# Kernel optimization log

Measured on AMD Instinct MI355X. Metric: run time of the kernel, lower is better.

## Reference

```python
import jax, jax.numpy as jnp
import numpy as np

N = 20000
E = 320000
CIN = 16
COUT = 16
D = 4
RADIUS = 0.5


def setup_inputs() -> dict:
    key = jax.random.key(0)
    k1, k2, k3, k4 = jax.random.split(key, 4)
    positions = jax.random.uniform(k1, (N, 3), dtype=jnp.float32)
    features = jax.random.normal(k2, (N, CIN), dtype=jnp.float32)
    filters = jax.random.normal(k3, (D, D, D, CIN, COUT), dtype=jnp.float32)
    edge_index = jax.random.randint(k4, (2, E), 0, N, dtype=jnp.int32)
    return {"positions": positions, "features": features,
            "filters": filters, "edge_index": edge_index}


def _trilinear(filters, gc):
    # Replicates torch grid_sample(align_corners=True) semantics used by the
    # module: grid coord (x,y,z) indexes spatial dims (W,H,D), i.e. gc[:,0]
    # samples filter axis 2, gc[:,1] axis 1, gc[:,2] axis 0.
    Dres = filters.shape[0]
    a, b, c = gc[:, 2], gc[:, 1], gc[:, 0]  # axes 0, 1, 2 of filters
    a0f, b0f, c0f = jnp.floor(a), jnp.floor(b), jnp.floor(c)
    a0 = jnp.clip(a0f.astype(jnp.int32), 0, Dres - 1)
    b0 = jnp.clip(b0f.astype(jnp.int32), 0, Dres - 1)
    c0 = jnp.clip(c0f.astype(jnp.int32), 0, Dres - 1)
    a1 = jnp.minimum(a0 + 1, Dres - 1)
    b1 = jnp.minimum(b0 + 1, Dres - 1)
    c1 = jnp.minimum(c0 + 1, Dres - 1)
    ad = (a - a0f)[:, None, None]  # (E,1,1)
    bd = (b - b0f)[:, None, None]
    cd = (c - c0f)[:, None, None]

    g = lambda i, j, k: filters[i, j, k]  # (E, CIN, COUT) gather
    f00 = g(a0, b0, c0) * (1 - cd) + g(a0, b0, c1) * cd
    f01 = g(a0, b1, c0) * (1 - cd) + g(a0, b1, c1) * cd
    f10 = g(a1, b0, c0) * (1 - cd) + g(a1, b0, c1) * cd
    f11 = g(a1, b1, c0) * (1 - cd) + g(a1, b1, c1) * cd
    f0 = f00 * (1 - bd) + f01 * bd
    f1 = f10 * (1 - bd) + f11 * bd
    return f0 * (1 - ad) + f1 * ad  # (E, CIN, COUT)


def reference(positions, features, filters, edge_index):
    row, col = edge_index[0], edge_index[1]
    r = positions[col] - positions[row]                  # (E,3)
    dist2 = jnp.sum(r * r, axis=-1)                      # (E,)
    valid = (dist2 < RADIUS ** 2).astype(positions.dtype)
    window = (1.0 - dist2 / RADIUS ** 2) ** 3 * valid
    norm = jnp.sqrt(dist2)[:, None]
    mapped = r / (norm + 1e-8) * jnp.tanh(norm)          # ball -> cube, (E,3)
    gc = (mapped + 1.0) * ((filters.shape[0] - 1) / 2.0) # (E,3) in [0, D-1]
    filt = _trilinear(filters, gc)                       # (E, CIN, COUT)
    conv_edge = jnp.einsum('eio,ei->eo', filt, features[col])
    conv_edge = conv_edge * window[:, None]
    n_nodes = positions.shape[0]
    sums = jax.ops.segment_sum(conv_edge, row, num_segments=n_nodes)
    cnt = jax.ops.segment_sum(jnp.ones((conv_edge.shape[0],), positions.dtype),
                              row, num_segments=n_nodes)
    return sums / jnp.maximum(cnt, 1.0)[:, None]         # scatter-mean
```

## Files before the change

### kernel.cpp

```cpp
#include <hip/hip_runtime.h>
#include <hip/hip_fp16.h>
#include <math.h>

#define NN 20000
#define EE 320000
#define CIN 16
#define COUT 16
#define R2C 0.25f
#define MAXDEG 32

#define CONV_OFF 81920

typedef _Float16 h2 __attribute__((ext_vector_type(2)));

#if defined(__has_builtin)
# if __has_builtin(__builtin_amdgcn_fdot2)
#  define HAS_FDOT2 1
# endif
#endif
#ifndef HAS_FDOT2
# define HAS_FDOT2 0
#endif

__device__ __forceinline__ h2 as_h2(unsigned int x) {
    union { unsigned int u; h2 h; } v; v.u = x; return v.h;
}
__device__ __forceinline__ h2 pk(float a, float b) {
    h2 r; r.x = (_Float16)a; r.y = (_Float16)b; return r;
}

__global__ __launch_bounds__(256) void k_zcnt(int* __restrict__ cnts) {
    int t = blockIdx.x * 256 + threadIdx.x;
    if (t < NN) cnts[t] = 0;
}

__global__ __launch_bounds__(256) void k_edge(const float* __restrict__ pos,
                                              const int* __restrict__ ei,
                                              const float* __restrict__ feat,
                                              const float* __restrict__ filt,
                                              float* __restrict__ conv,
                                              int* __restrict__ cnts) {
    __shared__ uint4 sf[2048];
    {
        __half* sh = (__half*)sf;
        const float4* f4 = (const float4*)filt;
        #pragma unroll
        for (int r = 0; r < 16; ++r) {
            int q = r * 256 + threadIdx.x;
            float4 v = f4[q];
            int cell = q >> 6;
            int ci   = (q >> 2) & 15;
            int o0   = (q & 3) << 2;
            int gb   = cell * 32 + (ci >> 3) * 16 + o0;
            int sl   = ci & 7;
            sh[(gb + 0) * 8 + sl] = __float2half(v.x);
            sh[(gb + 1) * 8 + sl] = __float2half(v.y);
            sh[(gb + 2) * 8 + sl] = __float2half(v.z);
            sh[(gb + 3) * 8 + sl] = __float2half(v.w);
        }
    }
    __syncthreads();

    int lane = threadIdx.x & 63;
    int gid  = lane >> 4;
    int o    = lane & 15;
    int e = (blockIdx.x * 4 + (threadIdx.x >> 6)) * 64 + lane;

    int row = ei[e];
    int col = ei[EE + e];

    float rx = pos[col*3+0] - pos[row*3+0];
    float ry = pos[col*3+1] - pos[row*3+1];
    float rz = pos[col*3+2] - pos[row*3+2];
    float d2 = rx*rx + ry*ry + rz*rz;
    bool valid = d2 < R2C;

    int old = atomicAdd(&cnts[row], valid ? 0x10001 : 1);

    float win = 0.f, ad = 0.f, bd = 0.f, cd = 0.f;
    int colidx = 0, rowslot = 0;
    if (valid) {
        float u = 1.0f - d2 * 4.0f;
        win = u * u * u;
        float s = 1.0f + d2*(-0.33333333f + d2*(0.13333333f + d2*(-0.05396825f + d2*0.02186949f)));
        float gx = (rx * s + 1.0f) * 1.5f;
        float gy = (ry * s + 1.0f) * 1.5f;
        float gz = (rz * s + 1.0f) * 1.5f;
        float af = floorf(gz), bf = floorf(gy), cf = floorf(gx);
        int ia0 = min(max((int)af, 0), 2);
        int jb0 = min(max((int)bf, 0), 2);
        int kc0 = min(max((int)cf, 0), 2);
        ad = gz - af; bd = gy - bf; cd = gx - cf;
        colidx  = col | (ia0 << 20) | (jb0 << 24) | (kc0 << 28);
        int slot = old >> 16;
        rowslot = row | (min(slot, MAXDEG) << 16);
    }

    unsigned long long bal = __ballot(valid);
    int nv = __popcll(bal);
    unsigned long long m0 = bal;
    unsigned long long m1 = m0 & (m0 - 1);
    unsigned long long m2 = m1 & (m1 - 1);
    unsigned long long m3 = m2 & (m2 - 1);

    for (int k = 0; k < nv; k += 4) {
        unsigned long long mg = (gid == 0) ? m0 : (gid == 1) ? m1 : (gid == 2) ? m2 : m3;
        bool active = (k + gid) < nv;
        int src = active ? (int)__builtin_ctzll(mg) : 0;

        float win_s = __shfl(win, src, 64);
        float ad_s  = __shfl(ad,  src, 64);
        float bd_s  = __shfl(bd,  src, 64);
        float cd_s  = __shfl(cd,  src, 64);
        int   ci_s  = __shfl(colidx,  src, 64);
        int   rs_s  = __shfl(rowslot, src, 64);

        m0 = m3 & (m3 - 1);
        m1 = m0 & (m0 - 1);
        m2 = m1 & (m1 - 1);
        m3 = m2 & (m2 - 1);

        if (active) {
            int col_s  = ci_s & 0xFFFFF;
            int ia0 = (ci_s >> 20) & 3, jb0 = (ci_s >> 24) & 3, kc0 = (ci_s >> 28) & 3;
            int row_s  = rs_s & 0xFFFF;
            int slot_s = rs_s >> 16;

            const float4* fb = (const float4*)(feat + (size_t)col_s * 16);
            float4 fa = fb[0], fc = fb[1], fd = fb[2], fe = fb[3];

            float va0 = (1.f - ad_s) * win_s, va1 = ad_s * win_s;
            float vb0 = 1.f - bd_s, vb1 = bd_s;
            float vc0 = 1.f - cd_s, vc1 = cd_s;
            float p00 = va0*vb0, p01 = va0*vb1, p10 = va1*vb0, p11 = va1*vb1;
            float w8[8] = { p00*vc0, p00*vc1, p01*vc0, p01*vc1,
                            p10*vc0, p10*vc1, p11*vc0, p11*vc1 };

            int bi = ((ia0 * 16 + jb0 * 4 + kc0) << 5) + o;
            const int cofs[8] = {0, 32, 128, 160, 512, 544, 640, 672};

            float acc = 0.f;
#if HAS_FDOT2
            h2 ft0 = pk(fa.x, fa.y), ft1 = pk(fa.z, fa.w);
            h2 ft2 = pk(fc.x, fc.y), ft3 = pk(fc.z, fc.w);
            h2 ft4 = pk(fd.x, fd.y), ft5 = pk(fd.z, fd.w);
            h2 ft6 = pk(fe.x, fe.y), ft7 = pk(fe.z, fe.w);
            #pragma unroll
            for (int c = 0; c < 8; ++c) {
                uint4 g0 = sf[bi + cofs[c]];
                uint4 g1 = sf[bi + cofs[c] + 16];
                float d = 0.f;
                d = __builtin_amdgcn_fdot2(as_h2(g0.x), ft0, d, false);
                d = __builtin_amdgcn_fdot2(as_h2(g0.y), ft1, d, false);
                d = __builtin_amdgcn_fdot2(as_h2(g0.z), ft2, d, false);
                d = __builtin_amdgcn_fdot2(as_h2(g0.w), ft3, d, false);
                d = __builtin_amdgcn_fdot2(as_h2(g1.x), ft4, d, false);
                d = __builtin_amdgcn_fdot2(as_h2(g1.y), ft5, d, false);
                d = __builtin_amdgcn_fdot2(as_h2(g1.z), ft6, d, false);
                d = __builtin_amdgcn_fdot2(as_h2(g1.w), ft7, d, false);
                acc = fmaf(w8[c], d, acc);
            }
#else
            float ftf[16] = { fa.x, fa.y, fa.z, fa.w, fc.x, fc.y, fc.z, fc.w,
                              fd.x, fd.y, fd.z, fd.w, fe.x, fe.y, fe.z, fe.w };
            #pragma unroll
            for (int c = 0; c < 8; ++c) {
                uint4 g0 = sf[bi + cofs[c]];
                uint4 g1 = sf[bi + cofs[c] + 16];
                float d = 0.f;
                h2 t;
                t = as_h2(g0.x); d = fmaf((float)t.x, ftf[0],  d); d = fmaf((float)t.y, ftf[1],  d);
                t = as_h2(g0.y); d = fmaf((float)t.x, ftf[2],  d); d = fmaf((float)t.y, ftf[3],  d);
                t = as_h2(g0.z); d = fmaf((float)t.x, ftf[4],  d); d = fmaf((float)t.y, ftf[5],  d);
                t = as_h2(g0.w); d = fmaf((float)t.x, ftf[6],  d); d = fmaf((float)t.y, ftf[7],  d);
                t = as_h2(g1.x); d = fmaf((float)t.x, ftf[8],  d); d = fmaf((float)t.y, ftf[9],  d);
                t = as_h2(g1.y); d = fmaf((float)t.x, ftf[10], d); d = fmaf((float)t.y, ftf[11], d);
                t = as_h2(g1.z); d = fmaf((float)t.x, ftf[12], d); d = fmaf((float)t.y, ftf[13], d);
                t = as_h2(g1.w); d = fmaf((float)t.x, ftf[14], d); d = fmaf((float)t.y, ftf[15], d);
                acc = fmaf(w8[c], d, acc);
            }
#endif
            if (slot_s < MAXDEG)
                conv[((size_t)row_s * MAXDEG + slot_s) * 16 + o] = acc;
        }
    }
}

__global__ __launch_bounds__(256) void k_gather(const float* __restrict__ conv,
                                                const int* __restrict__ cnts,
                                                float* __restrict__ out) {
    int t = blockIdx.x * 256 + threadIdx.x;
    int n = t >> 3;
    int h = t & 7;
    if (n >= NN) return;
    int p   = cnts[n];
    int deg = min(p >> 16, MAXDEG);
    int ca  = p & 0xFFFF;
    float2 acc = make_float2(0.f, 0.f);
    const float2* base = (const float2*)(conv + (size_t)n * MAXDEG * 16) + h;
    for (int s = 0; s < deg; ++s) {
        float2 q = base[(size_t)s * 8];
        acc.x += q.x;
        acc.y += q.y;
    }
    float inv = 1.0f / (float)max(ca, 1);
    *(float2*)(out + (size_t)n * 16 + h * 2) = make_float2(acc.x * inv, acc.y * inv);
}

__global__ __launch_bounds__(256) void k_zero(float* __restrict__ out, int* __restrict__ cnt) {
    int i = blockIdx.x * 256 + threadIdx.x;
    if (i < NN * COUT) out[i] = 0.0f;
    if (i < NN) cnt[i] = 0;
}

__device__ __forceinline__ bool edge_geom(const float* __restrict__ pos, int row, int col,
                                          float& win,
                                          int ia[2], int jb[2], int kc[2],
                                          float wa[2], float wb[2], float wc[2]) {
    float rx = pos[col*3+0] - pos[row*3+0];
    float ry = pos[col*3+1] - pos[row*3+1];
    float rz = pos[col*3+2] - pos[row*3+2];
    float d2 = rx*rx + ry*ry + rz*rz;
    if (!(d2 < R2C)) return false;
    float u = 1.0f - d2 / R2C;
    win = u * u * u;
    float nr = sqrtf(d2);
    float s  = tanhf(nr) / (nr + 1e-8f);
    float gx = (rx * s + 1.0f) * 1.5f;
    float gy = (ry * s + 1.0f) * 1.5f;
    float gz = (rz * s + 1.0f) * 1.5f;
    float af = floorf(gz), bf = floorf(gy), cf = floorf(gx);
    int ia0 = min(max((int)af, 0), 3);
    int ib0 = min(max((int)bf, 0), 3);
    int ic0 = min(max((int)cf, 0), 3);
    ia[0] = ia0; ia[1] = min(ia0 + 1, 3);
    jb[0] = ib0; jb[1] = min(ib0 + 1, 3);
    kc[0] = ic0; kc[1] = min(ic0 + 1, 3);
    float ad = gz - af, bd = gy - bf, cd = gx - cf;
    wa[0] = 1.0f - ad; wa[1] = ad;
    wb[0] = 1.0f - bd; wb[1] = bd;
    wc[0] = 1.0f - cd; wc[1] = cd;
    return true;
}

__global__ __launch_bounds__(256) void k_edge_direct(const float* __restrict__ pos,
                                                     const float* __restrict__ feat,
                                                     const float* __restrict__ filt,
                                                     const int* __restrict__ ei,
                                                     float* __restrict__ out,
                                                     int* __restrict__ cnt) {
    int e = blockIdx.x * 256 + threadIdx.x;
    if (e >= EE) return;
    int row = ei[e];
    int col = ei[EE + e];
    atomicAdd(&cnt[row], 1);

    float win;
    int ia[2], jb[2], kc[2];
    float wa[2], wb[2], wc[2];
    if (!edge_geom(pos, row, col, win, ia, jb, kc, wa, wb, wc)) return;

    float fv[16];
    const float4* fp = (const float4*)(feat + (size_t)col * 16);
    float4 f0 = fp[0], f1 = fp[1], f2 = fp[2], f3 = fp[3];
    fv[0]=f0.x; fv[1]=f0.y; fv[2]=f0.z; fv[3]=f0.w;
    fv[4]=f1.x; fv[5]=f1.y; fv[6]=f1.z; fv[7]=f1.w;
    fv[8]=f2.x; fv[9]=f2.y; fv[10]=f2.z; fv[11]=f2.w;
    fv[12]=f3.x; fv[13]=f3.y; fv[14]=f3.z; fv[15]=f3.w;

    float4 a0 = make_float4(0.f,0.f,0.f,0.f);
    float4 a1 = a0, a2 = a0, a3 = a0;
    for (int da = 0; da < 2; ++da)
    for (int db = 0; db < 2; ++db)
    for (int dc = 0; dc < 2; ++dc) {
        float w = wa[da] * wb[db] * wc[dc] * win;
        const float* fb = filt + (size_t)(ia[da]*16 + jb[db]*4 + kc[dc]) * 256;
        #pragma unroll
        for (int ci = 0; ci < 16; ++ci) {
            float c = w * fv[ci];
            const float4* r4 = (const float4*)(fb + ci * 16);
            float4 w0 = r4[0], w1 = r4[1], w2 = r4[2], w3 = r4[3];
            a0.x = fmaf(c, w0.x, a0.x); a0.y = fmaf(c, w0.y, a0.y);
            a0.z = fmaf(c, w0.z, a0.z); a0.w = fmaf(c, w0.w, a0.w);
            a1.x = fmaf(c, w1.x, a1.x); a1.y = fmaf(c, w1.y, a1.y);
            a1.z = fmaf(c, w1.z, a1.z); a1.w = fmaf(c, w1.w, a1.w);
            a2.x = fmaf(c, w2.x, a2.x); a2.y = fmaf(c, w2.y, a2.y);
            a2.z = fmaf(c, w2.z, a2.z); a2.w = fmaf(c, w2.w, a2.w);
            a3.x = fmaf(c, w3.x, a3.x); a3.y = fmaf(c, w3.y, a3.y);
            a3.z = fmaf(c, w3.z, a3.z); a3.w = fmaf(c, w3.w, a3.w);
        }
    }
    float* op = out + (size_t)row * 16;
    atomicAdd(op+0,  a0.x); atomicAdd(op+1,  a0.y); atomicAdd(op+2,  a0.z); atomicAdd(op+3,  a0.w);
    atomicAdd(op+4,  a1.x); atomicAdd(op+5,  a1.y); atomicAdd(op+6,  a1.z); atomicAdd(op+7,  a1.w);
    atomicAdd(op+8,  a2.x); atomicAdd(op+9,  a2.y); atomicAdd(op+10, a2.z); atomicAdd(op+11, a2.w);
    atomicAdd(op+12, a3.x); atomicAdd(op+13, a3.y); atomicAdd(op+14, a3.z); atomicAdd(op+15, a3.w);
}

__global__ __launch_bounds__(256) void k_div(float* __restrict__ out, const int* __restrict__ cnt) {
    int i = blockIdx.x * 256 + threadIdx.x;
    if (i >= NN * COUT) return;
    int c = cnt[i >> 4];
    float denom = (c > 1) ? (float)c : 1.0f;
    out[i] = out[i] / denom;
}

extern "C" void kernel_launch(void* const* d_in, const int* in_sizes, int n_in,
                              void* d_out, int out_size, void* d_ws, size_t ws_size,
                              hipStream_t stream) {
    const float* pos  = (const float*)d_in[0];
    const float* feat = (const float*)d_in[1];
    const float* filt = (const float*)d_in[2];
    const int*   ei   = (const int*)d_in[3];
    float* out = (float*)d_out;

    int*   cnts = (int*)d_ws;
    float* conv = (float*)((char*)d_ws + CONV_OFF);

    size_t need = (size_t)CONV_OFF + (size_t)NN * MAXDEG * 16 * sizeof(float);

    if (ws_size >= need) {
        k_zcnt<<<(NN + 255) / 256, 256, 0, stream>>>(cnts);
        k_edge<<<1250, 256, 0, stream>>>(pos, ei, feat, filt, conv, cnts);
        k_gather<<<(NN * 8 + 255) / 256, 256, 0, stream>>>(conv, cnts, out);
    } else {
        k_zero<<<(NN * COUT + 255) / 256, 256, 0, stream>>>(out, cnts);
        k_edge_direct<<<(EE + 255) / 256, 256, 0, stream>>>(pos, feat, filt, ei, out, cnts);
        k_div<<<(NN * COUT + 255) / 256, 256, 0, stream>>>(out, cnts);
    }
}
```

Baseline: 94.34 us.

## Replace slotted conv buffer and gather pass with direct atomic scatter

```diff
diff --git a/kernel.cpp b/kernel.cpp
--- a/kernel.cpp
+++ b/kernel.cpp
@@ -7,9 +7,8 @@
 #define CIN 16
 #define COUT 16
 #define R2C 0.25f
-#define MAXDEG 32
-
-#define CONV_OFF 81920
+
+#define WS_NEED 81920
 
 typedef _Float16 h2 __attribute__((ext_vector_type(2)));
 
@@ -28,35 +27,35 @@
 __device__ __forceinline__ h2 pk(float a, float b) {
     h2 r; r.x = (_Float16)a; r.y = (_Float16)b; return r;
 }
-
-__global__ __launch_bounds__(256) void k_zcnt(int* __restrict__ cnts) {
-    int t = blockIdx.x * 256 + threadIdx.x;
-    if (t < NN) cnts[t] = 0;
+__device__ __forceinline__ unsigned int pku(float a, float b) {
+    __half2 h = __float22half2_rn(make_float2(a, b));
+    return *(unsigned int*)&h;
+}
+
+__global__ __launch_bounds__(256) void k_zero(float* __restrict__ out, int* __restrict__ cnt) {
+    int i = blockIdx.x * 256 + threadIdx.x;
+    if (i < NN * COUT) out[i] = 0.0f;
+    if (i < NN) cnt[i] = 0;
 }
 
 __global__ __launch_bounds__(256) void k_edge(const float* __restrict__ pos,
                                               const int* __restrict__ ei,
                                               const float* __restrict__ feat,
                                               const float* __restrict__ filt,
-                                              float* __restrict__ conv,
+                                              float* __restrict__ out,
                                               int* __restrict__ cnts) {
     __shared__ uint4 sf[2048];
     {
-        __half* sh = (__half*)sf;
-        const float4* f4 = (const float4*)filt;
         #pragma unroll
-        for (int r = 0; r < 16; ++r) {
-            int q = r * 256 + threadIdx.x;
-            float4 v = f4[q];
-            int cell = q >> 6;
-            int ci   = (q >> 2) & 15;
-            int o0   = (q & 3) << 2;
-            int gb   = cell * 32 + (ci >> 3) * 16 + o0;
-            int sl   = ci & 7;
-            sh[(gb + 0) * 8 + sl] = __float2half(v.x);
-            sh[(gb + 1) * 8 + sl] = __float2half(v.y);
-            sh[(gb + 2) * 8 + sl] = __float2half(v.z);
-            sh[(gb + 3) * 8 + sl] = __float2half(v.w);
+        for (int r = 0; r < 8; ++r) {
+            int g = r * 256 + threadIdx.x;
+            const float* src = filt + (g >> 4) * 128 + (g & 15);
+            float s0 = src[0],  s1 = src[16],  s2 = src[32],  s3 = src[48];
+            float s4 = src[64], s5 = src[80],  s6 = src[96],  s7 = src[112];
+            uint4 v;
+            v.x = pku(s0, s1); v.y = pku(s2, s3);
+            v.z = pku(s4, s5); v.w = pku(s6, s7);
+            sf[g] = v;
         }
     }
     __syncthreads();
@@ -64,153 +63,133 @@
     int lane = threadIdx.x & 63;
     int gid  = lane >> 4;
     int o    = lane & 15;
-    int e = (blockIdx.x * 4 + (threadIdx.x >> 6)) * 64 + lane;
-
-    int row = ei[e];
-    int col = ei[EE + e];
-
-    float rx = pos[col*3+0] - pos[row*3+0];
-    float ry = pos[col*3+1] - pos[row*3+1];
-    float rz = pos[col*3+2] - pos[row*3+2];
-    float d2 = rx*rx + ry*ry + rz*rz;
-    bool valid = d2 < R2C;
-
-    int old = atomicAdd(&cnts[row], valid ? 0x10001 : 1);
-
-    float win = 0.f, ad = 0.f, bd = 0.f, cd = 0.f;
-    int colidx = 0, rowslot = 0;
-    if (valid) {
-        float u = 1.0f - d2 * 4.0f;
-        win = u * u * u;
-        float s = 1.0f + d2*(-0.33333333f + d2*(0.13333333f + d2*(-0.05396825f + d2*0.02186949f)));
-        float gx = (rx * s + 1.0f) * 1.5f;
-        float gy = (ry * s + 1.0f) * 1.5f;
-        float gz = (rz * s + 1.0f) * 1.5f;
-        float af = floorf(gz), bf = floorf(gy), cf = floorf(gx);
-        int ia0 = min(max((int)af, 0), 2);
-        int jb0 = min(max((int)bf, 0), 2);
-        int kc0 = min(max((int)cf, 0), 2);
-        ad = gz - af; bd = gy - bf; cd = gx - cf;
-        colidx  = col | (ia0 << 20) | (jb0 << 24) | (kc0 << 28);
-        int slot = old >> 16;
-        rowslot = row | (min(slot, MAXDEG) << 16);
-    }
-
-    unsigned long long bal = __ballot(valid);
-    int nv = __popcll(bal);
-    unsigned long long m0 = bal;
-    unsigned long long m1 = m0 & (m0 - 1);
-    unsigned long long m2 = m1 & (m1 - 1);
-    unsigned long long m3 = m2 & (m2 - 1);
-
-    for (int k = 0; k < nv; k += 4) {
-        unsigned long long mg = (gid == 0) ? m0 : (gid == 1) ? m1 : (gid == 2) ? m2 : m3;
-        bool active = (k + gid) < nv;
-        int src = active ? (int)__builtin_ctzll(mg) : 0;
-
-        float win_s = __shfl(win, src, 64);
-        float ad_s  = __shfl(ad,  src, 64);
-        float bd_s  = __shfl(bd,  src, 64);
-        float cd_s  = __shfl(cd,  src, 64);
-        int   ci_s  = __shfl(colidx,  src, 64);
-        int   rs_s  = __shfl(rowslot, src, 64);
-
-        m0 = m3 & (m3 - 1);
-        m1 = m0 & (m0 - 1);
-        m2 = m1 & (m1 - 1);
-        m3 = m2 & (m2 - 1);
-
-        if (active) {
-            int col_s  = ci_s & 0xFFFFF;
-            int ia0 = (ci_s >> 20) & 3, jb0 = (ci_s >> 24) & 3, kc0 = (ci_s >> 28) & 3;
-            int row_s  = rs_s & 0xFFFF;
-            int slot_s = rs_s >> 16;
-
-            const float4* fb = (const float4*)(feat + (size_t)col_s * 16);
-            float4 fa = fb[0], fc = fb[1], fd = fb[2], fe = fb[3];
-
-            float va0 = (1.f - ad_s) * win_s, va1 = ad_s * win_s;
-            float vb0 = 1.f - bd_s, vb1 = bd_s;
-            float vc0 = 1.f - cd_s, vc1 = cd_s;
-            float p00 = va0*vb0, p01 = va0*vb1, p10 = va1*vb0, p11 = va1*vb1;
-            float w8[8] = { p00*vc0, p00*vc1, p01*vc0, p01*vc1,
-                            p10*vc0, p10*vc1, p11*vc0, p11*vc1 };
-
-            int bi = ((ia0 * 16 + jb0 * 4 + kc0) << 5) + o;
-            const int cofs[8] = {0, 32, 128, 160, 512, 544, 640, 672};
-
-            float acc = 0.f;
+    int wv   = threadIdx.x >> 6;
+
+    #pragma unroll
+    for (int ch = 0; ch < 2; ++ch) {
+        int e = blockIdx.x * 512 + ch * 256 + wv * 64 + lane;
+
+        int row = ei[e];
+        int col = ei[EE + e];
+        atomicAdd(&cnts[row], 1);
+
+        float rx = pos[col*3+0] - pos[row*3+0];
+        float ry = pos[col*3+1] - pos[row*3+1];
+        float rz = pos[col*3+2] - pos[row*3+2];
+        float d2 = rx*rx + ry*ry + rz*rz;
+        bool valid = d2 < R2C;
+
+        float win = 0.f, ad = 0.f, bd = 0.f, cd = 0.f;
+        int colidx = 0;
+        if (valid) {
+            float u = 1.0f - d2 * 4.0f;
+            win = u * u * u;
+            float s = 1.0f + d2*(-0.33333333f + d2*(0.13333333f + d2*(-0.05396825f + d2*0.02186949f)));
+            float gx = (rx * s + 1.0f) * 1.5f;
+            float gy = (ry * s + 1.0f) * 1.5f;
+            float gz = (rz * s + 1.0f) * 1.5f;
+            float af = floorf(gz), bf = floorf(gy), cf = floorf(gx);
+            int ia0 = min(max((int)af, 0), 2);
+            int jb0 = min(max((int)bf, 0), 2);
+            int kc0 = min(max((int)cf, 0), 2);
+            ad = gz - af; bd = gy - bf; cd = gx - cf;
+            colidx = col | (ia0 << 20) | (jb0 << 24) | (kc0 << 28);
+        }
+
+        unsigned long long bal = __ballot(valid);
+        int nv = __popcll(bal);
+        unsigned long long m0 = bal;
+        unsigned long long m1 = m0 & (m0 - 1);
+        unsigned long long m2 = m1 & (m1 - 1);
+        unsigned long long m3 = m2 & (m2 - 1);
+
+        for (int k = 0; k < nv; k += 4) {
+            unsigned long long mg = (gid == 0) ? m0 : (gid == 1) ? m1 : (gid == 2) ? m2 : m3;
+            bool active = (k + gid) < nv;
+            int src = active ? (int)__builtin_ctzll(mg) : 0;
+
+            float win_s = __shfl(win, src, 64);
+            float ad_s  = __shfl(ad,  src, 64);
+            float bd_s  = __shfl(bd,  src, 64);
+            float cd_s  = __shfl(cd,  src, 64);
+            int   ci_s  = __shfl(colidx, src, 64);
+            int   row_s = __shfl(row,    src, 64);
+
+            m0 = m3 & (m3 - 1);
+            m1 = m0 & (m0 - 1);
+            m2 = m1 & (m1 - 1);
+            m3 = m2 & (m2 - 1);
+
+            if (active) {
+                int col_s = ci_s & 0xFFFFF;
+                int ia0 = (ci_s >> 20) & 3, jb0 = (ci_s >> 24) & 3, kc0 = (ci_s >> 28) & 3;
+
+                const float4* fb = (const float4*)(feat + (size_t)col_s * 16);
+                float4 fa = fb[0], fc = fb[1], fd = fb[2], fe = fb[3];
+
+                float va0 = (1.f - ad_s) * win_s, va1 = ad_s * win_s;
+                float vb0 = 1.f - bd_s, vb1 = bd_s;
+                float vc0 = 1.f - cd_s, vc1 = cd_s;
+                float p00 = va0*vb0, p01 = va0*vb1, p10 = va1*vb0, p11 = va1*vb1;
+                float w8[8] = { p00*vc0, p00*vc1, p01*vc0, p01*vc1,
+                                p10*vc0, p10*vc1, p11*vc0, p11*vc1 };
+
+                int bi = ((ia0 * 16 + jb0 * 4 + kc0) << 5) + o;
+                const int cofs[8] = {0, 32, 128, 160, 512, 544, 640, 672};
+
+                float acc = 0.f;
 #if HAS_FDOT2
-            h2 ft0 = pk(fa.x, fa.y), ft1 = pk(fa.z, fa.w);
-            h2 ft2 = pk(fc.x, fc.y), ft3 = pk(fc.z, fc.w);
-            h2 ft4 = pk(fd.x, fd.y), ft5 = pk(fd.z, fd.w);
-            h2 ft6 = pk(fe.x, fe.y), ft7 = pk(fe.z, fe.w);
-            #pragma unroll
-            for (int c = 0; c < 8; ++c) {
-                uint4 g0 = sf[bi + cofs[c]];
-                uint4 g1 = sf[bi + cofs[c] + 16];
-                float d = 0.f;
-                d = __builtin_amdgcn_fdot2(as_h2(g0.x), ft0, d, false);
-                d = __builtin_amdgcn_fdot2(as_h2(g0.y), ft1, d, false);
-                d = __builtin_amdgcn_fdot2(as_h2(g0.z), ft2, d, false);
-                d = __builtin_amdgcn_fdot2(as_h2(g0.w), ft3, d, false);
-                d = __builtin_amdgcn_fdot2(as_h2(g1.x), ft4, d, false);
-                d = __builtin_amdgcn_fdot2(as_h2(g1.y), ft5, d, false);
-                d = __builtin_amdgcn_fdot2(as_h2(g1.z), ft6, d, false);
-                d = __builtin_amdgcn_fdot2(as_h2(g1.w), ft7, d, false);
-                acc = fmaf(w8[c], d, acc);
+                h2 ft0 = pk(fa.x, fa.y), ft1 = pk(fa.z, fa.w);
+                h2 ft2 = pk(fc.x, fc.y), ft3 = pk(fc.z, fc.w);
+                h2 ft4 = pk(fd.x, fd.y), ft5 = pk(fd.z, fd.w);
+                h2 ft6 = pk(fe.x, fe.y), ft7 = pk(fe.z, fe.w);
+                #pragma unroll
+                for (int c = 0; c < 8; ++c) {
+                    uint4 g0 = sf[bi + cofs[c]];
+                    uint4 g1 = sf[bi + cofs[c] + 16];
+                    float d = 0.f;
+                    d = __builtin_amdgcn_fdot2(as_h2(g0.x), ft0, d, false);
+                    d = __builtin_amdgcn_fdot2(as_h2(g0.y), ft1, d, false);
+                    d = __builtin_amdgcn_fdot2(as_h2(g0.z), ft2, d, false);
+                    d = __builtin_amdgcn_fdot2(as_h2(g0.w), ft3, d, false);
+                    d = __builtin_amdgcn_fdot2(as_h2(g1.x), ft4, d, false);
+                    d = __builtin_amdgcn_fdot2(as_h2(g1.y), ft5, d, false);
+                    d = __builtin_amdgcn_fdot2(as_h2(g1.z), ft6, d, false);
+                    d = __builtin_amdgcn_fdot2(as_h2(g1.w), ft7, d, false);
+                    acc = fmaf(w8[c], d, acc);
+                }
+#else
+                float ftf[16] = { fa.x, fa.y, fa.z, fa.w, fc.x, fc.y, fc.z, fc.w,
+                                  fd.x, fd.y, fd.z, fd.w, fe.x, fe.y, fe.z, fe.w };
+                #pragma unroll
+                for (int c = 0; c < 8; ++c) {
+                    uint4 g0 = sf[bi + cofs[c]];
+                    uint4 g1 = sf[bi + cofs[c] + 16];
+                    float d = 0.f;
+                    h2 t;
+                    t = as_h2(g0.x); d = fmaf((float)t.x, ftf[0],  d); d = fmaf((float)t.y, ftf[1],  d);
+                    t = as_h2(g0.y); d = fmaf((float)t.x, ftf[2],  d); d = fmaf((float)t.y, ftf[3],  d);
+                    t = as_h2(g0.z); d = fmaf((float)t.x, ftf[4],  d); d = fmaf((float)t.y, ftf[5],  d);
+                    t = as_h2(g0.w); d = fmaf((float)t.x, ftf[6],  d); d = fmaf((float)t.y, ftf[7],  d);
+                    t = as_h2(g1.x); d = fmaf((float)t.x, ftf[8],  d); d = fmaf((float)t.y, ftf[9],  d);
+                    t = as_h2(g1.y); d = fmaf((float)t.x, ftf[10], d); d = fmaf((float)t.y, ftf[11], d);
+                    t = as_h2(g1.z); d = fmaf((float)t.x, ftf[12], d); d = fmaf((float)t.y, ftf[13], d);
+                    t = as_h2(g1.w); d = fmaf((float)t.x, ftf[14], d); d = fmaf((float)t.y, ftf[15], d);
+                    acc = fmaf(w8[c], d, acc);
+                }
+#endif
+                atomicAdd(out + (size_t)row_s * 16 + o, acc);
             }
-#else
-            float ftf[16] = { fa.x, fa.y, fa.z, fa.w, fc.x, fc.y, fc.z, fc.w,
-                              fd.x, fd.y, fd.z, fd.w, fe.x, fe.y, fe.z, fe.w };
-            #pragma unroll
-            for (int c = 0; c < 8; ++c) {
-                uint4 g0 = sf[bi + cofs[c]];
-                uint4 g1 = sf[bi + cofs[c] + 16];
-                float d = 0.f;
-                h2 t;
-                t = as_h2(g0.x); d = fmaf((float)t.x, ftf[0],  d); d = fmaf((float)t.y, ftf[1],  d);
-                t = as_h2(g0.y); d = fmaf((float)t.x, ftf[2],  d); d = fmaf((float)t.y, ftf[3],  d);
-                t = as_h2(g0.z); d = fmaf((float)t.x, ftf[4],  d); d = fmaf((float)t.y, ftf[5],  d);
-                t = as_h2(g0.w); d = fmaf((float)t.x, ftf[6],  d); d = fmaf((float)t.y, ftf[7],  d);
-                t = as_h2(g1.x); d = fmaf((float)t.x, ftf[8],  d); d = fmaf((float)t.y, ftf[9],  d);
-                t = as_h2(g1.y); d = fmaf((float)t.x, ftf[10], d); d = fmaf((float)t.y, ftf[11], d);
-                t = as_h2(g1.z); d = fmaf((float)t.x, ftf[12], d); d = fmaf((float)t.y, ftf[13], d);
-                t = as_h2(g1.w); d = fmaf((float)t.x, ftf[14], d); d = fmaf((float)t.y, ftf[15], d);
-                acc = fmaf(w8[c], d, acc);
-            }
-#endif
-            if (slot_s < MAXDEG)
-                conv[((size_t)row_s * MAXDEG + slot_s) * 16 + o] = acc;
-        }
-    }
-}
-
-__global__ __launch_bounds__(256) void k_gather(const float* __restrict__ conv,
-                                                const int* __restrict__ cnts,
-                                                float* __restrict__ out) {
-    int t = blockIdx.x * 256 + threadIdx.x;
-    int n = t >> 3;
-    int h = t & 7;
-    if (n >= NN) return;
-    int p   = cnts[n];
-    int deg = min(p >> 16, MAXDEG);
-    int ca  = p & 0xFFFF;
-    float2 acc = make_float2(0.f, 0.f);
-    const float2* base = (const float2*)(conv + (size_t)n * MAXDEG * 16) + h;
-    for (int s = 0; s < deg; ++s) {
-        float2 q = base[(size_t)s * 8];
-        acc.x += q.x;
-        acc.y += q.y;
-    }
-    float inv = 1.0f / (float)max(ca, 1);
-    *(float2*)(out + (size_t)n * 16 + h * 2) = make_float2(acc.x * inv, acc.y * inv);
-}
-
-__global__ __launch_bounds__(256) void k_zero(float* __restrict__ out, int* __restrict__ cnt) {
+        }
+    }
+}
+
+__global__ __launch_bounds__(256) void k_div(float* __restrict__ out, const int* __restrict__ cnt) {
     int i = blockIdx.x * 256 + threadIdx.x;
-    if (i < NN * COUT) out[i] = 0.0f;
-    if (i < NN) cnt[i] = 0;
+    if (i >= NN * COUT) return;
+    int c = cnt[i >> 4];
+    float denom = (c > 1) ? (float)c : 1.0f;
+    out[i] = out[i] / denom;
 }
 
 __device__ __forceinline__ bool edge_geom(const float* __restrict__ pos, int row, int col,
@@ -297,14 +276,6 @@
     atomicAdd(op+12, a3.x); atomicAdd(op+13, a3.y); atomicAdd(op+14, a3.z); atomicAdd(op+15, a3.w);
 }
 
-__global__ __launch_bounds__(256) void k_div(float* __restrict__ out, const int* __restrict__ cnt) {
-    int i = blockIdx.x * 256 + threadIdx.x;
-    if (i >= NN * COUT) return;
-    int c = cnt[i >> 4];
-    float denom = (c > 1) ? (float)c : 1.0f;
-    out[i] = out[i] / denom;
-}
-
 extern "C" void kernel_launch(void* const* d_in, const int* in_sizes, int n_in,
                               void* d_out, int out_size, void* d_ws, size_t ws_size,
                               hipStream_t stream) {
@@ -314,18 +285,13 @@
     const int*   ei   = (const int*)d_in[3];
     float* out = (float*)d_out;
 
-    int*   cnts = (int*)d_ws;
-    float* conv = (float*)((char*)d_ws + CONV_OFF);
-
-    size_t need = (size_t)CONV_OFF + (size_t)NN * MAXDEG * 16 * sizeof(float);
-
-    if (ws_size >= need) {
-        k_zcnt<<<(NN + 255) / 256, 256, 0, stream>>>(cnts);
-        k_edge<<<1250, 256, 0, stream>>>(pos, ei, feat, filt, conv, cnts);
-        k_gather<<<(NN * 8 + 255) / 256, 256, 0, stream>>>(conv, cnts, out);
+    int* cnts = (int*)d_ws;
+
+    k_zero<<<(NN * COUT + 255) / 256, 256, 0, stream>>>(out, cnts);
+    if (ws_size >= WS_NEED) {
+        k_edge<<<625, 256, 0, stream>>>(pos, ei, feat, filt, out, cnts);
     } else {
-        k_zero<<<(NN * COUT + 255) / 256, 256, 0, stream>>>(out, cnts);
         k_edge_direct<<<(EE + 255) / 256, 256, 0, stream>>>(pos, feat, filt, ei, out, cnts);
-        k_div<<<(NN * COUT + 255) / 256, 256, 0, stream>>>(out, cnts);
-    }
-}
+    }
+    k_div<<<(NN * COUT + 255) / 256, 256, 0, stream>>>(out, cnts);
+}
```

Measured after the change: 92.02 us. 1.03x faster.
